# Performance work log

Hardware: AMD Instinct MI355X
Metric: run time of the kernel (lower is better)

## Reference

```python
import jax, jax.numpy as jnp
import numpy as np

N = 30000      # nodes
E = 300000     # random edges (self-loops appended in setup)
B = 256        # graphs in batch
DIN = 128      # node_in_dim
H = 4          # heads (hardcoded in module)
C = 64         # gat_hidden_channels
D = H * C      # 256
DCLS = 768     # biobert cls dim
NC = 5         # num_classes


def setup_inputs() -> dict:
    ks = iter(jax.random.split(jax.random.key(0), 64))
    def rn(shape, s=0.05):
        return jax.random.normal(next(ks), shape, dtype=jnp.float32) * s
    inp = {}
    inp["x"] = jax.random.normal(next(ks), (N, DIN), jnp.float32)
    inp["biobert_cls"] = jax.random.normal(next(ks), (B, DCLS), jnp.float32)
    for i, din in zip((1, 2, 3), (DIN, D, D)):
        inp["g%d_wl" % i] = rn((din, D)); inp["g%d_bl" % i] = jnp.zeros((D,), jnp.float32)
        inp["g%d_wr" % i] = rn((din, D)); inp["g%d_br" % i] = jnp.zeros((D,), jnp.float32)
        inp["g%d_att" % i] = rn((H, C)); inp["g%d_bias" % i] = jnp.zeros((D,), jnp.float32)
        inp["bn%d_g" % i] = jnp.ones((D,), jnp.float32); inp["bn%d_b" % i] = jnp.zeros((D,), jnp.float32)
    inp["ca_wq"] = rn((D, D));    inp["ca_bq"] = jnp.zeros((D,), jnp.float32)
    inp["ca_wk"] = rn((DCLS, D)); inp["ca_bk"] = jnp.zeros((D,), jnp.float32)
    inp["ca_wv"] = rn((DCLS, D)); inp["ca_bv"] = jnp.zeros((D,), jnp.float32)
    inp["ca_wo"] = rn((D, D));    inp["ca_bo"] = jnp.zeros((D,), jnp.float32)
    inp["ca_ln_g"] = jnp.ones((D,), jnp.float32); inp["ca_ln_b"] = jnp.zeros((D,), jnp.float32)
    inp["ffn_w1"] = rn((D, D)); inp["ffn_b1"] = jnp.zeros((D,), jnp.float32)
    inp["ffn_w2"] = rn((D, D)); inp["ffn_b2"] = jnp.zeros((D,), jnp.float32)
    inp["fc_w"] = rn((D, NC)); inp["fc_b"] = jnp.zeros((NC,), jnp.float32)
    inp["fn_g"] = jnp.ones((D,), jnp.float32); inp["fn_b"] = jnp.zeros((D,), jnp.float32)
    src = jax.random.randint(next(ks), (E,), 0, N)
    dst = jax.random.randint(next(ks), (E,), 0, N)
    loop = jnp.arange(N)  # self-loops (PyG GATv2Conv default add_self_loops=True)
    inp["edge_src"] = jnp.concatenate([src, loop]).astype(jnp.int32)
    inp["edge_dst"] = jnp.concatenate([dst, loop]).astype(jnp.int32)
    inp["batch"] = jnp.sort(jax.random.randint(next(ks), (N,), 0, B)).astype(jnp.int32)
    return inp


def _gatv2(h, src, dst, wl, bl, wr, br, att, bias):
    # PyG GATv2Conv: e_ij = att . LeakyReLU(Wl x_j + Wr x_i); softmax over incoming edges of i
    n = h.shape[0]
    xl = (h @ wl + bl).reshape(n, H, C)
    xr = (h @ wr + br).reshape(n, H, C)
    e = jax.nn.leaky_relu(xl[src] + xr[dst], 0.2)          # [E,H,C]
    logit = jnp.einsum('ehc,hc->eh', e, att)                # [E,H]
    m = jax.ops.segment_max(logit, dst, num_segments=n)     # stable segment softmax
    a = jnp.exp(logit - m[dst])
    z = jax.ops.segment_sum(a, dst, num_segments=n)
    alpha = a / (z[dst] + 1e-16)
    out = jax.ops.segment_sum(xl[src] * alpha[:, :, None], dst, num_segments=n)
    return out.reshape(n, D) + bias


def _bn(x, g, b):
    m = x.mean(0); v = x.var(0)
    return (x - m) * jax.lax.rsqrt(v + 1e-5) * g + b


def _ln(x, g, b):
    m = x.mean(-1, keepdims=True); v = x.var(-1, keepdims=True)
    return (x - m) * jax.lax.rsqrt(v + 1e-5) * g + b


def reference(x, biobert_cls,
              g1_wl, g1_bl, g1_wr, g1_br, g1_att, g1_bias, bn1_g, bn1_b,
              g2_wl, g2_bl, g2_wr, g2_br, g2_att, g2_bias, bn2_g, bn2_b,
              g3_wl, g3_bl, g3_wr, g3_br, g3_att, g3_bias, bn3_g, bn3_b,
              ca_wq, ca_bq, ca_wk, ca_bk, ca_wv, ca_bv, ca_wo, ca_bo, ca_ln_g, ca_ln_b,
              ffn_w1, ffn_b1, ffn_w2, ffn_b2, fc_w, fc_b, fn_g, fn_b,
              edge_src, edge_dst, batch):
    h = jax.nn.elu(_bn(_gatv2(x, edge_src, edge_dst, g1_wl, g1_bl, g1_wr, g1_br, g1_att, g1_bias), bn1_g, bn1_b))
    h = jax.nn.elu(_bn(_gatv2(h, edge_src, edge_dst, g2_wl, g2_bl, g2_wr, g2_br, g2_att, g2_bias), bn2_g, bn2_b))
    h = jax.nn.elu(_bn(_gatv2(h, edge_src, edge_dst, g3_wl, g3_bl, g3_wr, g3_br, g3_att, g3_bias), bn3_g, bn3_b))
    # global add + mean pool, averaged
    add = jax.ops.segment_sum(h, batch, num_segments=B)                              # [B,D]
    cnt = jax.ops.segment_sum(jnp.ones((h.shape[0], 1), h.dtype), batch, num_segments=B)
    mean = add / jnp.maximum(cnt, 1.0)
    nf = (add + mean) * 0.5                                                           # [B,D]
    # multi-view cross attention (query seq len = 1, one biobert CLS key/value)
    hd = C
    Q = (nf @ ca_wq + ca_bq).reshape(B, 1, H, hd)
    K = (biobert_cls @ ca_wk + ca_bk).reshape(B, 1, H, hd)
    V = (biobert_cls @ ca_wv + ca_bv).reshape(B, 1, H, hd)
    scores = jnp.einsum('bqhd,bkhd->bhqk', Q, K) / jnp.sqrt(jnp.float32(hd))
    w = jax.nn.softmax(scores, axis=-1)
    ctx = jnp.einsum('bhqk,bkhd->bqhd', w, V).reshape(B, 1, D)
    ctx = _ln(ctx @ ca_wo + ca_bo, ca_ln_g, ca_ln_b)
    ffn = jax.nn.relu(ctx @ ffn_w1 + ffn_b1) @ ffn_w2 + ffn_b2
    out = _ln(ctx + ffn, fn_g, fn_b)
    logits = (out @ fc_w + fc_b)[:, 0, :]   # squeeze(1) -> [B, NC]
    return logits
```

## Files before the change

kernel.cpp:

```cpp
#include <hip/hip_runtime.h>
#include <math.h>


#define WV_ELEMS   (768 * 256)
#define W256_ELEMS (256 * 256)

__device__ __forceinline__ unsigned short f2bf_rne(float x) {
    unsigned u = __float_as_uint(x);
    unsigned r = (u + 0x7fffu + ((u >> 16) & 1u)) >> 16;
    return (unsigned short)r;
}
__device__ __forceinline__ float bf_lo(unsigned u) { return __uint_as_float(u << 16); }
__device__ __forceinline__ float bf_hi(unsigned u) { return __uint_as_float(u & 0xffff0000u); }

__global__ __launch_bounds__(256)
void cvt_weights(const float* __restrict__ wv, const float* __restrict__ wo,
                 const float* __restrict__ w1, const float* __restrict__ w2,
                 unsigned short* __restrict__ dst) {
    int i = blockIdx.x * 256 + threadIdx.x;
    const float4* src; int li;
    if (i < 49152)      { src = (const float4*)wv; li = i; }
    else if (i < 65536) { src = (const float4*)wo; li = i - 49152; }
    else if (i < 81920) { src = (const float4*)w1; li = i - 65536; }
    else                { src = (const float4*)w2; li = i - 81920; }
    float4 v = src[li];
    ushort4 o;
    o.x = f2bf_rne(v.x); o.y = f2bf_rne(v.y); o.z = f2bf_rne(v.z); o.w = f2bf_rne(v.w);
    ((ushort4*)dst)[i] = o;
}

__device__ __forceinline__ void ln_stats(float x, int tid, float* sred,
                                         float& m, float& rs) {
    float sum = x, sq = x * x;
    #pragma unroll
    for (int o = 32; o > 0; o >>= 1) {
        sum += __shfl_down(sum, o);
        sq  += __shfl_down(sq,  o);
    }
    const int lane = tid & 63, w = tid >> 6;
    if (lane == 0 && w < 4) { sred[w] = sum; sred[4 + w] = sq; }
    __syncthreads();
    if (tid == 0) {
        float S = sred[0] + sred[1] + sred[2] + sred[3];
        float Q = sred[4] + sred[5] + sred[6] + sred[7];
        float mm  = S * (1.0f / 256.0f);
        float var = Q * (1.0f / 256.0f) - mm * mm;
        sred[0] = mm;
        sred[1] = rsqrtf(fmaxf(var, 0.0f) + 1e-5f);
    }
    __syncthreads();
    m  = sred[0];
    rs = sred[1];
    __syncthreads();
}

__global__ __launch_bounds__(1024)
void mlp_head_kernel(const float* __restrict__ bio,
                     const unsigned short* __restrict__ wpack,
                     const float* __restrict__ bv, const float* __restrict__ bo,
                     const float* __restrict__ lng, const float* __restrict__ lnb,
                     const float* __restrict__ b1, const float* __restrict__ b2,
                     const float* __restrict__ fng, const float* __restrict__ fnb,
                     const float* __restrict__ fcw, const float* __restrict__ fcb,
                     float* __restrict__ out)
{
    const int b   = blockIdx.x;
    const int tid = threadIdx.x;
    const int q   = tid >> 6;
    const int co  = tid & 63;

    const unsigned short* wv16 = wpack;
    const unsigned short* wo16 = wpack + WV_ELEMS;
    const unsigned short* w116 = wo16 + W256_ELEMS;
    const unsigned short* w216 = w116 + W256_ELEMS;

    __shared__ float s_bio[768];
    __shared__ float s_act[256];
    __shared__ float s_part[16][256];
    __shared__ float s_red[8];

    if (tid < 768) s_bio[tid] = bio[b * 768 + tid];
    __syncthreads();

    #define GEMM_BF16(W16, KG, SRC) {                                         \
        float4 a0 = {0, 0, 0, 0};                                             \
        const uint2* wp = (const uint2*)(W16) + (q * (KG)) * 64 + co;         \
        const float* x0 = (SRC) + q * (KG);                                   \
        _Pragma("unroll 16")                                                  \
        for (int k = 0; k < (KG); ++k) {                                      \
            uint2 u = wp[k * 64];                                             \
            float v0 = x0[k];                                                 \
            a0.x = fmaf(v0, bf_lo(u.x), a0.x);                                \
            a0.y = fmaf(v0, bf_hi(u.x), a0.y);                                \
            a0.z = fmaf(v0, bf_lo(u.y), a0.z);                                \
            a0.w = fmaf(v0, bf_hi(u.y), a0.w);                                \
        }                                                                     \
        ((float4*)s_part[q])[co] = a0;                                        \
    }                                                                         \
    __syncthreads();

    #define REDUCE1(V) {                                                      \
        float p_ = 0.f;                                                       \
        _Pragma("unroll")                                                     \
        for (int g = 0; g < 16; ++g) p_ += s_part[g][tid];                    \
        V = p_;                                                               \
    }

    GEMM_BF16(wv16, 48, s_bio);
    if (tid < 256) {
        float p; REDUCE1(p);
        s_act[tid] = p + bv[tid];
    }
    __syncthreads();

    float ctx = 0.f;
    GEMM_BF16(wo16, 16, s_act);
    {
        float t = 0.f;
        if (tid < 256) {
            float p; REDUCE1(p);
            t = p + bo[tid];
        }
        float m, rs;
        ln_stats(t, tid, s_red, m, rs);
        if (tid < 256) {
            ctx = (t - m) * rs * lng[tid] + lnb[tid];
            s_act[tid] = ctx;
        }
    }
    __syncthreads();

    GEMM_BF16(w116, 16, s_act);
    if (tid < 256) {
        float p; REDUCE1(p);
        s_act[tid] = fmaxf(p + b1[tid], 0.0f);
    }
    __syncthreads();

    GEMM_BF16(w216, 16, s_act);
    {
        float o = 0.f;
        if (tid < 256) {
            float p; REDUCE1(p);
            o = p + b2[tid] + ctx;
        }
        float m, rs;
        ln_stats(o, tid, s_red, m, rs);
        if (tid < 256) s_act[tid] = (o - m) * rs * fng[tid] + fnb[tid];
    }
    __syncthreads();

    if (q == 0) {
        float acc[5] = {0, 0, 0, 0, 0};
        #pragma unroll
        for (int e = 0; e < 4; ++e) {
            int k = co + 64 * e;
            float xv = s_act[k];
            #pragma unroll
            for (int c = 0; c < 5; ++c) acc[c] = fmaf(xv, fcw[k * 5 + c], acc[c]);
        }
        #pragma unroll
        for (int o2 = 32; o2 > 0; o2 >>= 1) {
            #pragma unroll
            for (int c = 0; c < 5; ++c) acc[c] += __shfl_down(acc[c], o2);
        }
        if (co == 0) {
            #pragma unroll
            for (int c = 0; c < 5; ++c) out[b * 5 + c] = acc[c] + fcb[c];
        }
    }
    #undef GEMM_BF16
    #undef REDUCE1
}

extern "C" void kernel_launch(void* const* d_in, const int* in_sizes, int n_in,
                              void* d_out, int out_size, void* d_ws, size_t ws_size,
                              hipStream_t stream) {
    const float* bio = (const float*)d_in[1];
    const float* wv  = (const float*)d_in[30];
    const float* bv  = (const float*)d_in[31];
    const float* wo  = (const float*)d_in[32];
    const float* bo  = (const float*)d_in[33];
    const float* lng = (const float*)d_in[34];
    const float* lnb = (const float*)d_in[35];
    const float* w1  = (const float*)d_in[36];
    const float* b1  = (const float*)d_in[37];
    const float* w2  = (const float*)d_in[38];
    const float* b2  = (const float*)d_in[39];
    const float* fcw = (const float*)d_in[40];
    const float* fcb = (const float*)d_in[41];
    const float* fng = (const float*)d_in[42];
    const float* fnb = (const float*)d_in[43];
    float* out = (float*)d_out;
    unsigned short* wpack = (unsigned short*)d_ws;

    hipLaunchKernelGGL(cvt_weights, dim3(384), dim3(256), 0, stream,
                       wv, wo, w1, w2, wpack);
    for (int rep = 0; rep < 3; ++rep) {
        hipLaunchKernelGGL(mlp_head_kernel, dim3(256), dim3(1024), 0, stream,
                           bio, wpack, bv, bo, lng, lnb, b1, b2,
                           fng, fnb, fcw, fcb, out);
    }
}
```

Measured before the change: 196.2 us.

## Drop redundant head launches, repack bf16 weights in k-pairs, prefetch into registers

The MLP head kernel was launched three times with identical output; it now runs once. The bf16 weight pack is reorganised so each uint4 holds two consecutive k rows for four columns, which halves the number of load instructions in the GEMV loops. The next layer's weights are loaded into registers while the current reduction and layer norm run. Barriers become a raw waitcnt plus s_barrier, one barrier in ln_stats is removed, and biases and fc weights are preloaded into registers or LDS. The register prefetch raises register pressure, and the hand-written barrier relies on LDS-only ordering.

```diff
diff --git a/kernel.cpp b/kernel.cpp
--- a/kernel.cpp
+++ b/kernel.cpp
@@ -2,8 +2,8 @@
 #include <math.h>
 
 
-#define WV_ELEMS   (768 * 256)
-#define W256_ELEMS (256 * 256)
+#define WV_U4   24576
+#define W256_U4 8192
 
 __device__ __forceinline__ unsigned short f2bf_rne(float x) {
     unsigned u = __float_as_uint(x);
@@ -12,21 +12,33 @@
 }
 __device__ __forceinline__ float bf_lo(unsigned u) { return __uint_as_float(u << 16); }
 __device__ __forceinline__ float bf_hi(unsigned u) { return __uint_as_float(u & 0xffff0000u); }
+__device__ __forceinline__ unsigned packbf(float e, float o) {
+    return (unsigned)f2bf_rne(e) | ((unsigned)f2bf_rne(o) << 16);
+}
+
+__device__ __forceinline__ void lds_barrier() {
+    asm volatile("s_waitcnt lgkmcnt(0)\n\ts_barrier" ::: "memory");
+}
 
 __global__ __launch_bounds__(256)
 void cvt_weights(const float* __restrict__ wv, const float* __restrict__ wo,
                  const float* __restrict__ w1, const float* __restrict__ w2,
-                 unsigned short* __restrict__ dst) {
+                 uint4* __restrict__ dst) {
     int i = blockIdx.x * 256 + threadIdx.x;
     const float4* src; int li;
-    if (i < 49152)      { src = (const float4*)wv; li = i; }
-    else if (i < 65536) { src = (const float4*)wo; li = i - 49152; }
-    else if (i < 81920) { src = (const float4*)w1; li = i - 65536; }
-    else                { src = (const float4*)w2; li = i - 81920; }
-    float4 v = src[li];
-    ushort4 o;
-    o.x = f2bf_rne(v.x); o.y = f2bf_rne(v.y); o.z = f2bf_rne(v.z); o.w = f2bf_rne(v.w);
-    ((ushort4*)dst)[i] = o;
+    if (i < 24576)      { src = (const float4*)wv; li = i; }
+    else if (i < 32768) { src = (const float4*)wo; li = i - 24576; }
+    else if (i < 40960) { src = (const float4*)w1; li = i - 32768; }
+    else                { src = (const float4*)w2; li = i - 40960; }
+    int kp = li >> 6, c4 = li & 63;
+    float4 r0 = src[(2 * kp) * 64 + c4];
+    float4 r1 = src[(2 * kp + 1) * 64 + c4];
+    uint4 o;
+    o.x = packbf(r0.x, r1.x);
+    o.y = packbf(r0.y, r1.y);
+    o.z = packbf(r0.z, r1.z);
+    o.w = packbf(r0.w, r1.w);
+    dst[i] = o;
 }
 
 __device__ __forceinline__ void ln_stats(float x, int tid, float* sred,
@@ -39,7 +51,7 @@
     }
     const int lane = tid & 63, w = tid >> 6;
     if (lane == 0 && w < 4) { sred[w] = sum; sred[4 + w] = sq; }
-    __syncthreads();
+    lds_barrier();
     if (tid == 0) {
         float S = sred[0] + sred[1] + sred[2] + sred[3];
         float Q = sred[4] + sred[5] + sred[6] + sred[7];
@@ -48,15 +60,14 @@
         sred[0] = mm;
         sred[1] = rsqrtf(fmaxf(var, 0.0f) + 1e-5f);
     }
-    __syncthreads();
+    lds_barrier();
     m  = sred[0];
     rs = sred[1];
-    __syncthreads();
 }
 
 __global__ __launch_bounds__(1024)
 void mlp_head_kernel(const float* __restrict__ bio,
-                     const unsigned short* __restrict__ wpack,
+                     const uint4* __restrict__ wpack,
                      const float* __restrict__ bv, const float* __restrict__ bo,
                      const float* __restrict__ lng, const float* __restrict__ lnb,
                      const float* __restrict__ b1, const float* __restrict__ b2,
@@ -68,37 +79,87 @@
     const int tid = threadIdx.x;
     const int q   = tid >> 6;
     const int co  = tid & 63;
-
-    const unsigned short* wv16 = wpack;
-    const unsigned short* wo16 = wpack + WV_ELEMS;
-    const unsigned short* w116 = wo16 + W256_ELEMS;
-    const unsigned short* w216 = w116 + W256_ELEMS;
-
-    __shared__ float s_bio[768];
-    __shared__ float s_act[256];
-    __shared__ float s_part[16][256];
-    __shared__ float s_red[8];
-
-    if (tid < 768) s_bio[tid] = bio[b * 768 + tid];
-    __syncthreads();
-
-    #define GEMM_BF16(W16, KG, SRC) {                                         \
-        float4 a0 = {0, 0, 0, 0};                                             \
-        const uint2* wp = (const uint2*)(W16) + (q * (KG)) * 64 + co;         \
-        const float* x0 = (SRC) + q * (KG);                                   \
-        _Pragma("unroll 16")                                                  \
-        for (int k = 0; k < (KG); ++k) {                                      \
-            uint2 u = wp[k * 64];                                             \
-            float v0 = x0[k];                                                 \
-            a0.x = fmaf(v0, bf_lo(u.x), a0.x);                                \
-            a0.y = fmaf(v0, bf_hi(u.x), a0.y);                                \
-            a0.z = fmaf(v0, bf_lo(u.y), a0.z);                                \
-            a0.w = fmaf(v0, bf_hi(u.y), a0.w);                                \
+    const int cc  = tid & 255;
+
+    const uint4* wv4 = wpack;
+    const uint4* wo4 = wpack + WV_U4;
+    const uint4* w14 = wo4 + W256_U4;
+    const uint4* w24 = w14 + W256_U4;
+
+    __shared__ __align__(16) float s_bio[768];
+    __shared__ __align__(16) float s_act[256];
+    __shared__ __align__(16) float s_part[16][256];
+    __shared__ float s_red[16];
+    __shared__ float s_fcw[1280];
+
+    uint4 w_pre[8];
+    {
+        const uint4* pp = wo4 + (q * 8) * 64 + co;
+        #pragma unroll
+        for (int t = 0; t < 8; ++t) w_pre[t] = pp[t * 64];
+        #pragma unroll
+        for (int t = 0; t < 8; ++t) asm volatile("" : "+v"(w_pre[t].x));
+    }
+    float bvv = bv[cc], bov = bo[cc], lngv = lng[cc], lnbv = lnb[cc];
+    float b1v = b1[cc], b2v = b2[cc], fngv = fng[cc], fnbv = fnb[cc];
+    float fb[5];
+    #pragma unroll
+    for (int c = 0; c < 5; ++c) fb[c] = fcb[c];
+
+    if (tid < 768) {
+        s_bio[tid] = bio[b * 768 + tid];
+    } else {
+        int t0 = tid - 768;
+        #pragma unroll
+        for (int e = 0; e < 5; ++e) s_fcw[t0 + 256 * e] = fcw[t0 + 256 * e];
+    }
+    lds_barrier();
+
+    {
+        float4 a = {0, 0, 0, 0};
+        const uint4* wp = wv4 + (q * 24) * 64 + co;
+        const float* x0 = s_bio + q * 48;
+        #pragma unroll 8
+        for (int kp = 0; kp < 24; ++kp) {
+            uint4 u = wp[kp * 64];
+            float xe = x0[2 * kp], xo = x0[2 * kp + 1];
+            a.x = fmaf(xe, bf_lo(u.x), a.x); a.x = fmaf(xo, bf_hi(u.x), a.x);
+            a.y = fmaf(xe, bf_lo(u.y), a.y); a.y = fmaf(xo, bf_hi(u.y), a.y);
+            a.z = fmaf(xe, bf_lo(u.z), a.z); a.z = fmaf(xo, bf_hi(u.z), a.z);
+            a.w = fmaf(xe, bf_lo(u.w), a.w); a.w = fmaf(xo, bf_hi(u.w), a.w);
+        }
+        ((float4*)s_part[q])[co] = a;
+    }
+    lds_barrier();
+    if (tid < 256) {
+        float p = 0.f;
+        #pragma unroll
+        for (int g = 0; g < 16; ++g) p += s_part[g][tid];
+        s_act[tid] = p + bvv;
+    }
+    lds_barrier();
+
+    #define GEMM_REG() {                                                      \
+        float4 a = {0, 0, 0, 0};                                              \
+        const float* x0 = s_act + q * 16;                                     \
+        _Pragma("unroll")                                                     \
+        for (int t = 0; t < 8; ++t) {                                         \
+            uint4 u = w_pre[t];                                               \
+            float xe = x0[2 * t], xo = x0[2 * t + 1];                         \
+            a.x = fmaf(xe, bf_lo(u.x), a.x); a.x = fmaf(xo, bf_hi(u.x), a.x); \
+            a.y = fmaf(xe, bf_lo(u.y), a.y); a.y = fmaf(xo, bf_hi(u.y), a.y); \
+            a.z = fmaf(xe, bf_lo(u.z), a.z); a.z = fmaf(xo, bf_hi(u.z), a.z); \
+            a.w = fmaf(xe, bf_lo(u.w), a.w); a.w = fmaf(xo, bf_hi(u.w), a.w); \
         }                                                                     \
-        ((float4*)s_part[q])[co] = a0;                                        \
-    }                                                                         \
-    __syncthreads();
-
+        ((float4*)s_part[q])[co] = a;                                         \
+    }
+    #define PREFETCH(BASE) {                                                  \
+        const uint4* pp = (BASE) + (q * 8) * 64 + co;                         \
+        _Pragma("unroll")                                                     \
+        for (int t = 0; t < 8; ++t) w_pre[t] = pp[t * 64];                    \
+        _Pragma("unroll")                                                     \
+        for (int t = 0; t < 8; ++t) asm volatile("" : "+v"(w_pre[t].x));      \
+    }
     #define REDUCE1(V) {                                                      \
         float p_ = 0.f;                                                       \
         _Pragma("unroll")                                                     \
@@ -106,49 +167,47 @@
         V = p_;                                                               \
     }
 
-    GEMM_BF16(wv16, 48, s_bio);
-    if (tid < 256) {
-        float p; REDUCE1(p);
-        s_act[tid] = p + bv[tid];
-    }
-    __syncthreads();
-
+    GEMM_REG();
+    PREFETCH(w14);
+    lds_barrier();
     float ctx = 0.f;
-    GEMM_BF16(wo16, 16, s_act);
     {
         float t = 0.f;
         if (tid < 256) {
             float p; REDUCE1(p);
-            t = p + bo[tid];
+            t = p + bov;
         }
         float m, rs;
         ln_stats(t, tid, s_red, m, rs);
         if (tid < 256) {
-            ctx = (t - m) * rs * lng[tid] + lnb[tid];
+            ctx = (t - m) * rs * lngv + lnbv;
             s_act[tid] = ctx;
         }
     }
-    __syncthreads();
-
-    GEMM_BF16(w116, 16, s_act);
+    lds_barrier();
+
+    GEMM_REG();
+    PREFETCH(w24);
+    lds_barrier();
     if (tid < 256) {
         float p; REDUCE1(p);
-        s_act[tid] = fmaxf(p + b1[tid], 0.0f);
-    }
-    __syncthreads();
-
-    GEMM_BF16(w216, 16, s_act);
+        s_act[tid] = fmaxf(p + b1v, 0.0f);
+    }
+    lds_barrier();
+
+    GEMM_REG();
+    lds_barrier();
     {
         float o = 0.f;
         if (tid < 256) {
             float p; REDUCE1(p);
-            o = p + b2[tid] + ctx;
+            o = p + b2v + ctx;
         }
         float m, rs;
-        ln_stats(o, tid, s_red, m, rs);
-        if (tid < 256) s_act[tid] = (o - m) * rs * fng[tid] + fnb[tid];
-    }
-    __syncthreads();
+        ln_stats(o, tid, s_red + 8, m, rs);
+        if (tid < 256) s_act[tid] = (o - m) * rs * fngv + fnbv;
+    }
+    lds_barrier();
 
     if (q == 0) {
         float acc[5] = {0, 0, 0, 0, 0};
@@ -157,7 +216,7 @@
             int k = co + 64 * e;
             float xv = s_act[k];
             #pragma unroll
-            for (int c = 0; c < 5; ++c) acc[c] = fmaf(xv, fcw[k * 5 + c], acc[c]);
+            for (int c = 0; c < 5; ++c) acc[c] = fmaf(xv, s_fcw[k * 5 + c], acc[c]);
         }
         #pragma unroll
         for (int o2 = 32; o2 > 0; o2 >>= 1) {
@@ -166,10 +225,11 @@
         }
         if (co == 0) {
             #pragma unroll
-            for (int c = 0; c < 5; ++c) out[b * 5 + c] = acc[c] + fcb[c];
-        }
-    }
-    #undef GEMM_BF16
+            for (int c = 0; c < 5; ++c) out[b * 5 + c] = acc[c] + fb[c];
+        }
+    }
+    #undef GEMM_REG
+    #undef PREFETCH
     #undef REDUCE1
 }
 
@@ -192,13 +252,11 @@
     const float* fng = (const float*)d_in[42];
     const float* fnb = (const float*)d_in[43];
     float* out = (float*)d_out;
-    unsigned short* wpack = (unsigned short*)d_ws;
-
-    hipLaunchKernelGGL(cvt_weights, dim3(384), dim3(256), 0, stream,
+    uint4* wpack = (uint4*)d_ws;
+
+    hipLaunchKernelGGL(cvt_weights, dim3(192), dim3(256), 0, stream,
                        wv, wo, w1, w2, wpack);
-    for (int rep = 0; rep < 3; ++rep) {
-        hipLaunchKernelGGL(mlp_head_kernel, dim3(256), dim3(1024), 0, stream,
-                           bio, wpack, bv, bo, lng, lnb, b1, b2,
-                           fng, fnb, fcw, fcb, out);
-    }
-}
+    hipLaunchKernelGGL(mlp_head_kernel, dim3(256), dim3(1024), 0, stream,
+                       bio, wpack, bv, bo, lng, lnb, b1, b2,
+                       fng, fnb, fcw, fcb, out);
+}
```

Measured after the change: 158.5 us. -19.2%, faster.
